# Kernel optimization log

Hardware: AMD Instinct MI355X
Metric: run time of the kernel (lower is better)

The kernel has to match this reference:

```python
import jax, jax.numpy as jnp
import numpy as np

TEMPERATURE = 0.1
EPS = 1e-8

# MatchingRuleAllViews defaults:
#   intra_view_same_class=1, intra_view_different_class=0,
#   inter_view_same_class=1, inter_view_different_class=0,
#   inter_image_same_class=-1, inter_image_different_class=-1,
#   self_similarity=-1

def setup_inputs() -> dict:
    key = jax.random.key(0)
    k1, k2, k3 = jax.random.split(key, 3)
    B, V, C, HW = 2, 2, 64, 1024
    student = jax.random.normal(k1, (B, V, C, HW), dtype=jnp.float32)
    teacher = jax.random.normal(k2, (B, V, C, HW), dtype=jnp.float32)
    labels = jax.random.randint(k3, (B, V, HW), 0, 5, dtype=jnp.int32)
    return {"student_embeddings": student, "teacher_embeddings": teacher, "labels": labels}


def _masks(B, V, HW, labels_flat):
    # image / view / pixel ids for each of the N = B*V*HW flattened positions
    image_ids = jnp.repeat(jnp.arange(B), V * HW)          # [N]
    view_ids = jnp.tile(jnp.repeat(jnp.arange(V), HW), B)  # [N]
    pixel_ids = jnp.tile(jnp.arange(HW), B * V)            # [N]
    si = image_ids[:, None] == image_ids[None, :]
    sv = view_ids[:, None] == view_ids[None, :]
    sp = pixel_ids[:, None] == pixel_ids[None, :]
    sc = labels_flat[:, None] == labels_flat[None, :]
    # default rule: same image -> (same class ? 1 : 0); different image -> -1;
    # self-similarity (same image, view, pixel) -> -1
    mask = jnp.where(si, jnp.where(sc, 1, 0), -1)
    mask = jnp.where(si & sv & sp, -1, mask)
    numerator_mask = (mask == 1).astype(jnp.float32)
    denom_mask = (mask >= 0).astype(jnp.float32)
    return numerator_mask, denom_mask


def reference(student_embeddings, teacher_embeddings, labels):
    B, V, C, HW = student_embeddings.shape
    N = B * V * HW
    # [B,V,C,HW] -> [N,C], L2-normalized
    sf = student_embeddings.transpose(0, 1, 3, 2).reshape(N, C)
    tf = teacher_embeddings.transpose(0, 1, 3, 2).reshape(N, C)
    sf = sf / jnp.linalg.norm(sf, axis=1, keepdims=True).clip(1e-12)
    tf = tf / jnp.linalg.norm(tf, axis=1, keepdims=True).clip(1e-12)
    logits = (sf @ tf.T) / TEMPERATURE  # [N,N]

    labels_flat = labels.reshape(-1)
    numerator_mask, denom_mask = _masks(B, V, HW, labels_flat)

    # masked log-softmax over dim 1 (denominator restricted to denom_mask)
    masked_logits = jnp.where(denom_mask > 0, logits, -jnp.inf)
    log_prob = jax.nn.log_softmax(masked_logits, axis=1)
    log_prob = jnp.where(jnp.isneginf(log_prob), 0.0, log_prob)

    numerator_sums = numerator_mask.sum(1)
    mean_log_prob_pos = (numerator_mask * log_prob).sum(1) / (numerator_sums + EPS)
    valid = numerator_sums > EPS  # [N] bool
    n_valid = valid.sum().astype(jnp.float32)
    loss = -jnp.sum(jnp.where(valid, mean_log_prob_pos, 0.0)) / n_valid

    # bg_anchors=False branch: (loss * non_bg[valid]).sum() / (non_bg[valid].sum() + eps)
    non_bg = (labels_flat != 0).astype(jnp.float32)
    non_bg_valid_sum = jnp.sum(non_bg * valid.astype(jnp.float32))
    loss = (loss * non_bg_valid_sum) / (non_bg_valid_sum + EPS)
    return loss
```

## Files before the change

### kernel.cpp

```cpp
#include <hip/hip_runtime.h>
#include <math.h>

#define C_DIM 64
#define NEG_INF (-1e30f)
#define AW 132
#define BW 140

__global__ __launch_bounds__(256, 2) void fused_scl_kernel(
    const float* __restrict__ s, const float* __restrict__ t,
    const int* __restrict__ labels, float4* __restrict__ stats) {

    const int rb = blockIdx.x >> 4;
    const int jc = blockIdx.x & 15;
    const int img = rb >> 4;
    const int i0 = rb * 128;
    const int jb = img * 2048 + jc * 128;

    const int tid = threadIdx.x;
    const int tx = tid & 15;
    const int ty = tid >> 4;

    __shared__ __align__(16) float lds_a[C_DIM][AW];
    __shared__ __align__(16) float lds_b[C_DIM][BW];
    __shared__ float lds_rs[128], lds_rt[128];
    __shared__ int lds_labi[128], lds_labj[128];

    if (tid < 128) lds_labi[tid] = labels[i0 + tid];
    else           lds_labj[tid - 128] = labels[jb + tid - 128];

    {
        const int pos4 = (tid & 31) << 2;
        const int c0 = tid >> 5;
        const int bvi = ((i0 >> 10) << 16) + (i0 & 1023) + pos4;
        const int bvj = ((jb >> 10) << 16) + (jb & 1023) + pos4;
        const int sp = pos4 + ((pos4 >> 5) << 2);
#pragma unroll
        for (int k = 0; k < 8; ++k) {
            int c = c0 + (k << 3);
            *(float4*)&lds_a[c][pos4] = *(const float4*)(s + bvi + c * 1024);
            *(float4*)&lds_b[c][sp]   = *(const float4*)(t + bvj + c * 1024);
        }
    }
    __syncthreads();

    {
        const int p = tid & 127;
        float ssq = 0.f;
        if (tid < 128) {
#pragma unroll
            for (int c = 0; c < C_DIM; ++c) {
                float v = lds_a[c][p];
                ssq = fmaf(v, v, ssq);
            }
            lds_rs[p] = 1.f / fmaxf(sqrtf(ssq), 1e-12f);
        } else {
            const int sp = p + ((p >> 5) << 2);
#pragma unroll
            for (int c = 0; c < C_DIM; ++c) {
                float v = lds_b[c][sp];
                ssq = fmaf(v, v, ssq);
            }
            lds_rt[p] = 1.f / fmaxf(sqrtf(ssq), 1e-12f);
        }
    }
    __syncthreads();

    const int arow = ty << 3;
    const int bo = tx << 3;
    const int bos = bo + ((bo >> 5) << 2);

    float acc[8][8];
#pragma unroll
    for (int a = 0; a < 8; ++a)
#pragma unroll
        for (int b = 0; b < 8; ++b) acc[a][b] = 0.f;

#pragma unroll 4
    for (int c = 0; c < C_DIM; ++c) {
        float4 a0 = *(const float4*)&lds_a[c][arow];
        float4 a1 = *(const float4*)&lds_a[c][arow + 4];
        float4 b0 = *(const float4*)&lds_b[c][bos];
        float4 b1 = *(const float4*)&lds_b[c][bos + 4];
        const float ar[8] = {a0.x, a0.y, a0.z, a0.w, a1.x, a1.y, a1.z, a1.w};
        const float br[8] = {b0.x, b0.y, b0.z, b0.w, b1.x, b1.y, b1.z, b1.w};
#pragma unroll
        for (int a = 0; a < 8; ++a)
#pragma unroll
            for (int b = 0; b < 8; ++b)
                acc[a][b] = fmaf(ar[a], br[b], acc[a][b]);
    }

    int labi[8]; float rsi[8];
#pragma unroll
    for (int rr = 0; rr < 8; ++rr) {
        labi[rr] = lds_labi[arow + rr];
        rsi[rr] = lds_rs[arow + rr] * 10.f;
    }
    int labj[8]; float rtj[8];
#pragma unroll
    for (int jj = 0; jj < 8; ++jj) {
        labj[jj] = lds_labj[bo + jj];
        rtj[jj] = lds_rt[bo + jj];
    }

    float m_run[8], s_run[8], A_run[8], c_run[8];
#pragma unroll
    for (int rr = 0; rr < 8; ++rr) {
        const int i_g = i0 + arow + rr;
        float vals[8];
        float lm = NEG_INF;
        float A = 0.f, cn = 0.f;
#pragma unroll
        for (int jj = 0; jj < 8; ++jj) {
            float logit = acc[rr][jj] * rsi[rr] * rtj[jj];
            bool self = ((jb + bo + jj) == i_g);
            float v = self ? NEG_INF : logit;
            vals[jj] = v;
            lm = fmaxf(lm, v);
            if (!self && labj[jj] == labi[rr]) { A += logit; cn += 1.f; }
        }
        float sn = 0.f;
#pragma unroll
        for (int jj = 0; jj < 8; ++jj) sn += __expf(vals[jj] - lm);
        m_run[rr] = lm; s_run[rr] = sn; A_run[rr] = A; c_run[rr] = cn;
    }

#pragma unroll
    for (int off = 1; off < 16; off <<= 1) {
#pragma unroll
        for (int rr = 0; rr < 8; ++rr) {
            float m2 = __shfl_xor(m_run[rr], off, 64);
            float s2 = __shfl_xor(s_run[rr], off, 64);
            float A2 = __shfl_xor(A_run[rr], off, 64);
            float c2 = __shfl_xor(c_run[rr], off, 64);
            float M = fmaxf(m_run[rr], m2);
            s_run[rr] = s_run[rr] * __expf(m_run[rr] - M) + s2 * __expf(m2 - M);
            m_run[rr] = M;
            A_run[rr] += A2;
            c_run[rr] += c2;
        }
    }

    if (tx == 0) {
#pragma unroll
        for (int rr = 0; rr < 8; ++rr)
            stats[(i0 + arow + rr) * 16 + jc] =
                make_float4(m_run[rr], s_run[rr], A_run[rr], c_run[rr]);
    }
}

__global__ __launch_bounds__(256) void finalize_kernel(
    const float4* __restrict__ stats, const int* __restrict__ labels,
    float* __restrict__ accums, float* __restrict__ out) {
    const int tid = threadIdx.x;
    const int r = blockIdx.x * 256 + tid;

    float m = NEG_INF, sexp = 0.f, A = 0.f, cnt = 0.f;
#pragma unroll
    for (int c = 0; c < 16; ++c) {
        float4 v = stats[r * 16 + c];
        float M = fmaxf(m, v.x);
        sexp = sexp * __expf(m - M) + v.y * __expf(v.x - M);
        m = M;
        A += v.z;
        cnt += v.w;
    }
    float mlpp = 0.f, val = 0.f, nbv = 0.f;
    if (cnt > 0.5f) {
        float lse = m + __logf(sexp);
        mlpp = (A - cnt * lse) / (cnt + 1e-8f);
        val = 1.f;
        nbv = (labels[r] != 0) ? 1.f : 0.f;
    }

    __shared__ float red0[256], red1[256], red2[256];
    red0[tid] = mlpp; red1[tid] = val; red2[tid] = nbv;
    __syncthreads();
    for (int off = 128; off > 0; off >>= 1) {
        if (tid < off) {
            red0[tid] += red0[tid + off];
            red1[tid] += red1[tid + off];
            red2[tid] += red2[tid + off];
        }
        __syncthreads();
    }

    if (tid == 0) {
        atomicAdd(&accums[0], red0[0]);
        atomicAdd(&accums[1], red1[0]);
        atomicAdd(&accums[2], red2[0]);
        __threadfence();
        unsigned int old = atomicAdd((unsigned int*)&accums[3], 1u);
        if (old == 15u) {
            float S = atomicAdd(&accums[0], 0.f);
            float V = atomicAdd(&accums[1], 0.f);
            float NB = atomicAdd(&accums[2], 0.f);
            float loss = -S / V;
            out[0] = loss * NB / (NB + 1e-8f);
        }
    }
}

extern "C" void kernel_launch(void* const* d_in, const int* in_sizes, int n_in,
                              void* d_out, int out_size, void* d_ws, size_t ws_size,
                              hipStream_t stream) {
    const float* s = (const float*)d_in[0];
    const float* t = (const float*)d_in[1];
    const int* labels = (const int*)d_in[2];
    float* out = (float*)d_out;

    float* accums = (float*)d_ws;
    float4* stats = (float4*)((char*)d_ws + 32);

    hipMemsetAsync(accums, 0, 32, stream);
    hipLaunchKernelGGL(fused_scl_kernel, dim3(512), dim3(256), 0, stream,
                       s, t, labels, stats);
    hipLaunchKernelGGL(finalize_kernel, dim3(16), dim3(256), 0, stream,
                       stats, labels, accums, out);
}
```

Baseline: 85.44 us.

## Use bf16 MFMA for similarity tile with fixed-max softmax and inline accum reset

Student and teacher tiles are converted to bf16 in row-major LDS, and the 128x128 dot-product tile is computed with the MFMA 16x16x32 bf16 instruction instead of scalar FP32 FMAs. Since normalized logits are bounded by 1/temperature, the online max tracking is replaced by a fixed offset of 10, which removes the max shuffles and rescaling exps. The memset is dropped and the accumulators are zeroed by block 0 of the first kernel. The cost is bf16 precision loss in the logits, plus reliance on the bound logits ≤ 10 holding.

```diff
diff --git a/kernel.cpp b/kernel.cpp
--- a/kernel.cpp
+++ b/kernel.cpp
@@ -1,14 +1,23 @@
 #include <hip/hip_runtime.h>
 #include <math.h>
 
-#define C_DIM 64
 #define NEG_INF (-1e30f)
-#define AW 132
-#define BW 140
+
+typedef __attribute__((ext_vector_type(8))) short s16x8;
+typedef __attribute__((ext_vector_type(4))) float f32x4;
+
+__device__ __forceinline__ unsigned int pack_bf16(float lo, float hi) {
+    unsigned int ul = __float_as_uint(lo);
+    ul += 0x7FFFu + ((ul >> 16) & 1u);
+    unsigned int uh = __float_as_uint(hi);
+    uh += 0x7FFFu + ((uh >> 16) & 1u);
+    return (ul >> 16) | (uh & 0xFFFF0000u);
+}
 
 __global__ __launch_bounds__(256, 2) void fused_scl_kernel(
     const float* __restrict__ s, const float* __restrict__ t,
-    const int* __restrict__ labels, float4* __restrict__ stats) {
+    const int* __restrict__ labels, float4* __restrict__ stats,
+    float* __restrict__ accums) {
 
     const int rb = blockIdx.x >> 4;
     const int jc = blockIdx.x & 15;
@@ -17,135 +26,142 @@
     const int jb = img * 2048 + jc * 128;
 
     const int tid = threadIdx.x;
-    const int tx = tid & 15;
-    const int ty = tid >> 4;
-
-    __shared__ __align__(16) float lds_a[C_DIM][AW];
-    __shared__ __align__(16) float lds_b[C_DIM][BW];
+
+    __shared__ __align__(16) short lds_a[128 * 72];
+    __shared__ __align__(16) short lds_b[128 * 72];
     __shared__ float lds_rs[128], lds_rt[128];
     __shared__ int lds_labi[128], lds_labj[128];
 
+    if (blockIdx.x == 0 && tid < 8) accums[tid] = 0.f;
+
     if (tid < 128) lds_labi[tid] = labels[i0 + tid];
     else           lds_labj[tid - 128] = labels[jb + tid - 128];
 
     {
-        const int pos4 = (tid & 31) << 2;
-        const int c0 = tid >> 5;
+        const int t7 = tid & 7;
+        const int pos4 = (tid >> 3) << 2;
         const int bvi = ((i0 >> 10) << 16) + (i0 & 1023) + pos4;
         const int bvj = ((jb >> 10) << 16) + (jb & 1023) + pos4;
-        const int sp = pos4 + ((pos4 >> 5) << 2);
-#pragma unroll
-        for (int k = 0; k < 8; ++k) {
-            int c = c0 + (k << 3);
-            *(float4*)&lds_a[c][pos4] = *(const float4*)(s + bvi + c * 1024);
-            *(float4*)&lds_b[c][sp]   = *(const float4*)(t + bvj + c * 1024);
+        unsigned int* wa = (unsigned int*)lds_a;
+        unsigned int* wb = (unsigned int*)lds_b;
+#pragma unroll
+        for (int k = 0; k < 4; ++k) {
+            const int c0 = 2 * t7 + 16 * k;
+            float4 a0 = *(const float4*)(s + bvi + c0 * 1024);
+            float4 a1 = *(const float4*)(s + bvi + (c0 + 1) * 1024);
+            float4 b0 = *(const float4*)(t + bvj + c0 * 1024);
+            float4 b1 = *(const float4*)(t + bvj + (c0 + 1) * 1024);
+            const int w = t7 + 8 * k;
+            wa[36 * (pos4 + 0) + w] = pack_bf16(a0.x, a1.x);
+            wa[36 * (pos4 + 1) + w] = pack_bf16(a0.y, a1.y);
+            wa[36 * (pos4 + 2) + w] = pack_bf16(a0.z, a1.z);
+            wa[36 * (pos4 + 3) + w] = pack_bf16(a0.w, a1.w);
+            wb[36 * (pos4 + 0) + w] = pack_bf16(b0.x, b1.x);
+            wb[36 * (pos4 + 1) + w] = pack_bf16(b0.y, b1.y);
+            wb[36 * (pos4 + 2) + w] = pack_bf16(b0.z, b1.z);
+            wb[36 * (pos4 + 3) + w] = pack_bf16(b0.w, b1.w);
         }
     }
     __syncthreads();
 
     {
-        const int p = tid & 127;
+        const int row = tid & 127;
+        const unsigned int* wr =
+            (const unsigned int*)((tid < 128) ? lds_a : lds_b) + 36 * row;
         float ssq = 0.f;
-        if (tid < 128) {
-#pragma unroll
-            for (int c = 0; c < C_DIM; ++c) {
-                float v = lds_a[c][p];
-                ssq = fmaf(v, v, ssq);
+#pragma unroll
+        for (int i = 0; i < 8; ++i) {
+            uint4 u4 = *(const uint4*)(wr + 4 * i);
+            const unsigned int uu[4] = {u4.x, u4.y, u4.z, u4.w};
+#pragma unroll
+            for (int q = 0; q < 4; ++q) {
+                float lo = __uint_as_float(uu[q] << 16);
+                float hi = __uint_as_float(uu[q] & 0xFFFF0000u);
+                ssq = fmaf(lo, lo, ssq);
+                ssq = fmaf(hi, hi, ssq);
             }
-            lds_rs[p] = 1.f / fmaxf(sqrtf(ssq), 1e-12f);
-        } else {
-            const int sp = p + ((p >> 5) << 2);
-#pragma unroll
-            for (int c = 0; c < C_DIM; ++c) {
-                float v = lds_b[c][sp];
-                ssq = fmaf(v, v, ssq);
+        }
+        float r = 1.f / fmaxf(sqrtf(ssq), 1e-12f);
+        if (tid < 128) lds_rs[row] = r;
+        else           lds_rt[row] = r;
+    }
+    __syncthreads();
+
+    const int lane = tid & 63;
+    const int wv = tid >> 6;
+    const int warow = wv << 5;
+    const int quad = lane >> 4;
+    const int col16 = lane & 15;
+
+    s16x8 afr[2][2];
+#pragma unroll
+    for (int rt2 = 0; rt2 < 2; ++rt2) {
+        const short* pa = lds_a + (warow + 16 * rt2 + col16) * 72 + 8 * quad;
+        afr[rt2][0] = *(const s16x8*)pa;
+        afr[rt2][1] = *(const s16x8*)(pa + 32);
+    }
+
+    f32x4 acc[2][8];
+#pragma unroll
+    for (int ct = 0; ct < 8; ++ct) {
+        const short* pb = lds_b + (16 * ct + col16) * 72 + 8 * quad;
+        s16x8 blo = *(const s16x8*)pb;
+        s16x8 bhi = *(const s16x8*)(pb + 32);
+#pragma unroll
+        for (int rt2 = 0; rt2 < 2; ++rt2) {
+            f32x4 z = {0.f, 0.f, 0.f, 0.f};
+            z = __builtin_amdgcn_mfma_f32_16x16x32_bf16(afr[rt2][0], blo, z, 0, 0, 0);
+            z = __builtin_amdgcn_mfma_f32_16x16x32_bf16(afr[rt2][1], bhi, z, 0, 0, 0);
+            acc[rt2][ct] = z;
+        }
+    }
+
+    float s_sum[8], A_sum[8], c_sum[8], rsi[8];
+    int labi[8], ig[8];
+#pragma unroll
+    for (int rt2 = 0; rt2 < 2; ++rt2)
+#pragma unroll
+        for (int reg = 0; reg < 4; ++reg) {
+            const int rr = rt2 * 4 + reg;
+            const int rloc = warow + 16 * rt2 + 4 * quad + reg;
+            rsi[rr] = lds_rs[rloc] * 10.f;
+            labi[rr] = lds_labi[rloc];
+            ig[rr] = i0 + rloc;
+            s_sum[rr] = 0.f; A_sum[rr] = 0.f; c_sum[rr] = 0.f;
+        }
+
+#pragma unroll
+    for (int ct = 0; ct < 8; ++ct) {
+        const int jg = jb + 16 * ct + col16;
+        const float rtj = lds_rt[16 * ct + col16];
+        const int lj = lds_labj[16 * ct + col16];
+#pragma unroll
+        for (int rt2 = 0; rt2 < 2; ++rt2)
+#pragma unroll
+            for (int reg = 0; reg < 4; ++reg) {
+                const int rr = rt2 * 4 + reg;
+                float logit = acc[rt2][ct][reg] * rsi[rr] * rtj;
+                bool self = (jg == ig[rr]);
+                float e = __expf((self ? NEG_INF : logit) - 10.f);
+                s_sum[rr] += e;
+                if (!self && lj == labi[rr]) { A_sum[rr] += logit; c_sum[rr] += 1.f; }
             }
-            lds_rt[p] = 1.f / fmaxf(sqrtf(ssq), 1e-12f);
-        }
-    }
-    __syncthreads();
-
-    const int arow = ty << 3;
-    const int bo = tx << 3;
-    const int bos = bo + ((bo >> 5) << 2);
-
-    float acc[8][8];
-#pragma unroll
-    for (int a = 0; a < 8; ++a)
-#pragma unroll
-        for (int b = 0; b < 8; ++b) acc[a][b] = 0.f;
-
-#pragma unroll 4
-    for (int c = 0; c < C_DIM; ++c) {
-        float4 a0 = *(const float4*)&lds_a[c][arow];
-        float4 a1 = *(const float4*)&lds_a[c][arow + 4];
-        float4 b0 = *(const float4*)&lds_b[c][bos];
-        float4 b1 = *(const float4*)&lds_b[c][bos + 4];
-        const float ar[8] = {a0.x, a0.y, a0.z, a0.w, a1.x, a1.y, a1.z, a1.w};
-        const float br[8] = {b0.x, b0.y, b0.z, b0.w, b1.x, b1.y, b1.z, b1.w};
-#pragma unroll
-        for (int a = 0; a < 8; ++a)
-#pragma unroll
-            for (int b = 0; b < 8; ++b)
-                acc[a][b] = fmaf(ar[a], br[b], acc[a][b]);
-    }
-
-    int labi[8]; float rsi[8];
-#pragma unroll
-    for (int rr = 0; rr < 8; ++rr) {
-        labi[rr] = lds_labi[arow + rr];
-        rsi[rr] = lds_rs[arow + rr] * 10.f;
-    }
-    int labj[8]; float rtj[8];
-#pragma unroll
-    for (int jj = 0; jj < 8; ++jj) {
-        labj[jj] = lds_labj[bo + jj];
-        rtj[jj] = lds_rt[bo + jj];
-    }
-
-    float m_run[8], s_run[8], A_run[8], c_run[8];
-#pragma unroll
-    for (int rr = 0; rr < 8; ++rr) {
-        const int i_g = i0 + arow + rr;
-        float vals[8];
-        float lm = NEG_INF;
-        float A = 0.f, cn = 0.f;
-#pragma unroll
-        for (int jj = 0; jj < 8; ++jj) {
-            float logit = acc[rr][jj] * rsi[rr] * rtj[jj];
-            bool self = ((jb + bo + jj) == i_g);
-            float v = self ? NEG_INF : logit;
-            vals[jj] = v;
-            lm = fmaxf(lm, v);
-            if (!self && labj[jj] == labi[rr]) { A += logit; cn += 1.f; }
-        }
-        float sn = 0.f;
-#pragma unroll
-        for (int jj = 0; jj < 8; ++jj) sn += __expf(vals[jj] - lm);
-        m_run[rr] = lm; s_run[rr] = sn; A_run[rr] = A; c_run[rr] = cn;
-    }
-
-#pragma unroll
-    for (int off = 1; off < 16; off <<= 1) {
+    }
+
+#pragma unroll
+    for (int off = 1; off < 16; off <<= 1)
 #pragma unroll
         for (int rr = 0; rr < 8; ++rr) {
-            float m2 = __shfl_xor(m_run[rr], off, 64);
-            float s2 = __shfl_xor(s_run[rr], off, 64);
-            float A2 = __shfl_xor(A_run[rr], off, 64);
-            float c2 = __shfl_xor(c_run[rr], off, 64);
-            float M = fmaxf(m_run[rr], m2);
-            s_run[rr] = s_run[rr] * __expf(m_run[rr] - M) + s2 * __expf(m2 - M);
-            m_run[rr] = M;
-            A_run[rr] += A2;
-            c_run[rr] += c2;
-        }
-    }
-
-    if (tx == 0) {
+            s_sum[rr] += __shfl_xor(s_sum[rr], off, 64);
+            A_sum[rr] += __shfl_xor(A_sum[rr], off, 64);
+            c_sum[rr] += __shfl_xor(c_sum[rr], off, 64);
+        }
+
+    if (col16 == 0) {
 #pragma unroll
         for (int rr = 0; rr < 8; ++rr)
-            stats[(i0 + arow + rr) * 16 + jc] =
-                make_float4(m_run[rr], s_run[rr], A_run[rr], c_run[rr]);
+            stats[ig[rr] * 16 + jc] =
+                make_float4(s_sum[rr], A_sum[rr], c_sum[rr], 0.f);
     }
 }
 
@@ -155,19 +171,15 @@
     const int tid = threadIdx.x;
     const int r = blockIdx.x * 256 + tid;
 
-    float m = NEG_INF, sexp = 0.f, A = 0.f, cnt = 0.f;
+    float ssum = 0.f, A = 0.f, cnt = 0.f;
 #pragma unroll
     for (int c = 0; c < 16; ++c) {
         float4 v = stats[r * 16 + c];
-        float M = fmaxf(m, v.x);
-        sexp = sexp * __expf(m - M) + v.y * __expf(v.x - M);
-        m = M;
-        A += v.z;
-        cnt += v.w;
+        ssum += v.x; A += v.y; cnt += v.z;
     }
     float mlpp = 0.f, val = 0.f, nbv = 0.f;
     if (cnt > 0.5f) {
-        float lse = m + __logf(sexp);
+        float lse = 10.f + __logf(ssum);
         mlpp = (A - cnt * lse) / (cnt + 1e-8f);
         val = 1.f;
         nbv = (labels[r] != 0) ? 1.f : 0.f;
@@ -212,9 +224,8 @@
     float* accums = (float*)d_ws;
     float4* stats = (float4*)((char*)d_ws + 32);
 
-    hipMemsetAsync(accums, 0, 32, stream);
     hipLaunchKernelGGL(fused_scl_kernel, dim3(512), dim3(256), 0, stream,
-                       s, t, labels, stats);
+                       s, t, labels, stats, accums);
     hipLaunchKernelGGL(finalize_kernel, dim3(16), dim3(256), 0, stream,
                        stats, labels, accums, out);
 }
```

Measured after the change: 74.21 us (median of 2 runs). 13.1% less time.
